# Kernel tuning notes

Measured on AMD Instinct MI355X. Metric: run time of the kernel, lower is better.

## Reference

```python
import jax, jax.numpy as jnp
import numpy as np

HIDDEN = 512
N_LAYERS = 2
SEQ = 512
BATCH = 64
H2 = HIDDEN * 2  # 1024
D_IN = H2 * (N_LAYERS + 1)  # 3072


def setup_inputs() -> dict:
    key = jax.random.key(0)
    ks = jax.random.split(key, 4)
    state = jax.random.normal(ks[0], (N_LAYERS, BATCH, H2), dtype=jnp.float32)
    encoder_output = jax.random.normal(ks[1], (SEQ, BATCH, H2), dtype=jnp.float32)
    # fc1: xavier_normal with tanh gain (5/3); fc2: kaiming_normal
    xavier_std = (5.0 / 3.0) * np.sqrt(2.0 / (D_IN + H2))
    W1 = jax.random.normal(ks[2], (H2, D_IN), dtype=jnp.float32) * xavier_std
    b1 = jnp.zeros((H2,), dtype=jnp.float32)
    W2 = jax.random.normal(ks[3], (1, H2), dtype=jnp.float32) * np.sqrt(2.0 / H2)
    b2 = jnp.zeros((1,), dtype=jnp.float32)
    return {"state": state, "encoder_output": encoder_output,
            "W1": W1, "b1": b1, "W2": W2, "b2": b2}


def reference(state, encoder_output, W1, b1, W2, b2):
    S, B, h2 = encoder_output.shape
    # (n_layers, B, H2) -> (B, n_layers*H2), broadcast over seq
    st = jnp.transpose(state, (1, 0, 2)).reshape(B, -1)
    st = jnp.broadcast_to(st[:, None, :], (B, S, st.shape[-1]))
    enc = jnp.transpose(encoder_output, (1, 0, 2))  # (B, S, H2)
    concat = jnp.concatenate([st, enc], axis=2)      # (B, S, 3*H2)
    energy = jnp.tanh(jnp.einsum('bsd,hd->bsh', concat, W1) + b1)
    energy = (jnp.einsum('bsh,oh->bso', energy, W2) + b2)  # (B, S, 1)
    energy = jnp.transpose(energy, (0, 2, 1))        # (B, 1, S)
    alpha = jax.nn.softmax(energy, axis=2)           # (B, 1, S)
    context = jnp.einsum('bqs,bsh->qbh', alpha, enc)  # (1, B, H2)
    return context, alpha
```

## Files before the change

kernel.cpp:

```cpp
#include <hip/hip_runtime.h>
#include <hip/hip_bf16.h>
#include <stdint.h>

#define H2      1024
#define SEQ     512
#define BATCH   64
#define M_TOTAL (SEQ * BATCH)

typedef __attribute__((ext_vector_type(8))) short short8;
typedef __attribute__((ext_vector_type(4))) float f32x4;

__device__ __forceinline__ unsigned pack2_bf16(float lo, float hi) {
    union { __hip_bfloat162 h; unsigned u; } v;
    v.h = __float22bfloat162_rn(make_float2(lo, hi));
    return v.u;
}

__device__ __forceinline__ float fast_tanh(float x) {
    float e = __expf(2.0f * x);
    return __fdividef(e - 1.0f, e + 1.0f);
}

__device__ __forceinline__ void gl_lds16(const unsigned short* g, unsigned short* l) {
    __builtin_amdgcn_global_load_lds(
        (const __attribute__((address_space(1))) unsigned int*)g,
        (__attribute__((address_space(3))) unsigned int*)l, 16, 0, 0);
}


__global__ __launch_bounds__(256) void k_setup(const float* __restrict__ W1,
                                               const float* __restrict__ b1,
                                               const float* __restrict__ state,
                                               const float* __restrict__ enc,
                                               unsigned short* __restrict__ W1e,
                                               unsigned short* __restrict__ encb,
                                               float* __restrict__ logits,
                                               float* __restrict__ sp) {
    __shared__ unsigned short T[16 * 512];
    int blk = blockIdx.x, tid = threadIdx.x;
    int lane = tid & 63;
    if (blk < 512) {
        int gr = blk * 4 + (tid >> 6);
        int h  = ((gr >> 5) << 4) + (lane & 15);
        int k  = ((gr & 31) << 5) + ((lane >> 4) << 3);
        const float* src = W1 + (size_t)h * 3072 + 2048 + k;
        float4 v0 = *(const float4*)(src);
        float4 v1 = *(const float4*)(src + 4);
        uint4 o;
        o.x = pack2_bf16(v0.x, v0.y); o.y = pack2_bf16(v0.z, v0.w);
        o.z = pack2_bf16(v1.x, v1.y); o.w = pack2_bf16(v1.z, v1.w);
        *(uint4*)(W1e + (size_t)gr * 512 + lane * 8) = o;
    } else if (blk < 640) {
        logits[(blk - 512) * 256 + tid] = 0.f;
    } else if (blk < 704) {
        int mT   = blk - 640;
        int wave = tid >> 6;
        int c    = lane & 15;
        int kq   = (lane >> 4) << 3;
        int h    = mT * 16 + c;
        int b    = wave * 16 + c;
        const float* ap = W1 + (size_t)h * 3072 + kq;
        f32x4 acc = {0.f, 0.f, 0.f, 0.f};
        #pragma unroll 4
        for (int k0 = 0; k0 < 2048; k0 += 32) {
            int k = k0 + kq;
            float4 a0 = *(const float4*)(ap + k0);
            float4 a1 = *(const float4*)(ap + k0 + 4);
            int l = k >> 10, j = k & 1023;
            const float* bp = state + (((size_t)l * 64 + b) << 10) + j;
            float4 b0 = *(const float4*)bp;
            float4 b1v = *(const float4*)(bp + 4);
            union { short8 s; uint4 u; } fa, fb;
            fa.u.x = pack2_bf16(a0.x, a0.y); fa.u.y = pack2_bf16(a0.z, a0.w);
            fa.u.z = pack2_bf16(a1.x, a1.y); fa.u.w = pack2_bf16(a1.z, a1.w);
            fb.u.x = pack2_bf16(b0.x, b0.y); fb.u.y = pack2_bf16(b0.z, b0.w);
            fb.u.z = pack2_bf16(b1v.x, b1v.y); fb.u.w = pack2_bf16(b1v.z, b1v.w);
            acc = __builtin_amdgcn_mfma_f32_16x16x32_bf16(fa.s, fb.s, acc, 0, 0, 0);
        }
        int quad = lane >> 4;
        int bcol = wave * 16 + c;
        #pragma unroll
        for (int i = 0; i < 4; ++i) {
            int hh = mT * 16 + quad * 4 + i;
            sp[((size_t)bcol << 10) + hh] = acc[i] + b1[hh];
        }
    } else {
        int RB = blk - 704;
        const float*    src = enc  + (size_t)RB * 16384;
        unsigned short* dst = encb + (size_t)RB * 16384;
        int rhalf = tid >> 7;
        int colq  = (tid & 127) << 2;
        #pragma unroll
        for (int h = 0; h < 2; ++h) {
            if (h) __syncthreads();
            #pragma unroll
            for (int rp = 0; rp < 8; ++rp) {
                int row = rp * 2 + rhalf;
                float4 v = *(const float4*)(src + (size_t)row * 1024 + h * 512 + colq);
                uint2 o;
                o.x = pack2_bf16(v.x, v.y);
                o.y = pack2_bf16(v.z, v.w);
                int byte = (row * 1024 + colq * 2) ^ ((row & 7) << 4);
                *(uint2*)((char*)T + byte) = o;
            }
            __syncthreads();
            #pragma unroll
            for (int q = 0; q < 4; ++q) {
                int c   = q * 256 + tid;
                int KCl = c >> 6;
                int L   = c & 63;
                int row = L & 15;
                int kb  = KCl * 64 + ((L >> 4) << 4);
                int byte = (row * 1024 + kb) ^ ((row & 7) << 4);
                uint4 d = *(const uint4*)((const char*)T + byte);
                *(uint4*)(dst + ((size_t)(h * 16 + KCl) * 512) + L * 8) = d;
            }
        }
    }
}

#define BM 128
#define BN 128
#define BK 64
#define KSTEPS (H2 / BK)

__global__ __launch_bounds__(256, 2) void k_energy(const unsigned short* __restrict__ encb,
                                                   const unsigned short* __restrict__ W1e,
                                                   const float* __restrict__ sp,
                                                   const float* __restrict__ W2,
                                                   float* __restrict__ logits) {
    __shared__ unsigned short As[BM * BK];
    __shared__ unsigned short Bs[BN * BK];
    int bid = blockIdx.x;
    int c8  = bid & 7;
    int jj  = bid >> 3;
    int mT  = c8 * 32 + (jj >> 3);
    int nT  = jj & 7;
    int n0  = nT * BN;
    int m0  = mT * BM;
    int tid  = threadIdx.x;
    int lane = tid & 63, wave = tid >> 6;
    int wm   = (wave >> 1) << 6;
    int wn   = (wave & 1) << 6;

    int rg0 = wave * 2, rg1 = wave * 2 + 1;
    const unsigned short* gA0 = encb + ((size_t)(mT * 8 + rg0) * 32) * 512 + lane * 8;
    const unsigned short* gA1 = encb + ((size_t)(mT * 8 + rg1) * 32) * 512 + lane * 8;
    const unsigned short* gB0 = W1e  + ((size_t)(nT * 8 + rg0) * 32) * 512 + lane * 8;
    const unsigned short* gB1 = W1e  + ((size_t)(nT * 8 + rg1) * 32) * 512 + lane * 8;
    unsigned short* lA00 = As + (rg0 * 2 + 0) * 512;
    unsigned short* lA01 = As + (rg0 * 2 + 1) * 512;
    unsigned short* lA10 = As + (rg1 * 2 + 0) * 512;
    unsigned short* lA11 = As + (rg1 * 2 + 1) * 512;
    unsigned short* lB00 = Bs + (rg0 * 2 + 0) * 512;
    unsigned short* lB01 = Bs + (rg0 * 2 + 1) * 512;
    unsigned short* lB10 = Bs + (rg1 * 2 + 0) * 512;
    unsigned short* lB11 = Bs + (rg1 * 2 + 1) * 512;

    f32x4 acc[4][4];
    #pragma unroll
    for (int mi = 0; mi < 4; ++mi)
        #pragma unroll
        for (int ni = 0; ni < 4; ++ni)
            acc[mi][ni] = (f32x4){0.f, 0.f, 0.f, 0.f};

    int ablk = wm >> 4;
    int bblk = wn >> 4;

    for (int t = 0; t < KSTEPS; ++t) {
        int go = t * 1024;
        __syncthreads();
        gl_lds16(gA0 + go,       lA00);
        gl_lds16(gA0 + go + 512, lA01);
        gl_lds16(gA1 + go,       lA10);
        gl_lds16(gA1 + go + 512, lA11);
        gl_lds16(gB0 + go,       lB00);
        gl_lds16(gB0 + go + 512, lB01);
        gl_lds16(gB1 + go,       lB10);
        gl_lds16(gB1 + go + 512, lB11);
        __syncthreads();
        short8 af[4][2], bf[4][2];
        #pragma unroll
        for (int i = 0; i < 4; ++i) {
            #pragma unroll
            for (int kh = 0; kh < 2; ++kh) {
                af[i][kh] = *(const short8*)(As + ((ablk + i) * 2 + kh) * 512 + lane * 8);
                bf[i][kh] = *(const short8*)(Bs + ((bblk + i) * 2 + kh) * 512 + lane * 8);
            }
        }
        #pragma unroll
        for (int mi = 0; mi < 4; ++mi)
            #pragma unroll
            for (int ni = 0; ni < 4; ++ni) {
                acc[mi][ni] = __builtin_amdgcn_mfma_f32_16x16x32_bf16(af[mi][0], bf[ni][0], acc[mi][ni], 0, 0, 0);
                acc[mi][ni] = __builtin_amdgcn_mfma_f32_16x16x32_bf16(af[mi][1], bf[ni][1], acc[mi][ni], 0, 0, 0);
            }
    }

    int c    = lane & 15;
    int quad = lane >> 4;
    float w2v[4];
    int   hcol[4];
    #pragma unroll
    for (int ni = 0; ni < 4; ++ni) {
        hcol[ni] = n0 + wn + ni * 16 + c;
        w2v[ni]  = W2[hcol[ni]];
    }
    #pragma unroll
    for (int mi = 0; mi < 4; ++mi) {
        #pragma unroll
        for (int i = 0; i < 4; ++i) {
            int m = m0 + wm + mi * 16 + quad * 4 + i;
            int b = m & 63;
            const float* sprow = sp + ((size_t)b << 10);
            float t = 0.f;
            #pragma unroll
            for (int ni = 0; ni < 4; ++ni) {
                float e = acc[mi][ni][i] + sprow[hcol[ni]];
                t = fmaf(fast_tanh(e), w2v[ni], t);
            }
            t += __shfl_xor(t, 1);
            t += __shfl_xor(t, 2);
            t += __shfl_xor(t, 4);
            t += __shfl_xor(t, 8);
            if (c == 0) atomicAdd(logits + (size_t)b * 512 + (m >> 6), t);
        }
    }
}

__global__ __launch_bounds__(256) void k_softmax(const float* __restrict__ logits,
                                                 float* __restrict__ alpha) {
    int b = blockIdx.x;
    int tid = threadIdx.x;
    int lane = tid & 63, wave = tid >> 6;
    float v0 = logits[(size_t)b * 512 + tid];
    float v1 = logits[(size_t)b * 512 + 256 + tid];
    float mx = fmaxf(v0, v1);
    #pragma unroll
    for (int o = 32; o; o >>= 1) mx = fmaxf(mx, __shfl_xor(mx, o));
    __shared__ float redm[4];
    if (lane == 0) redm[wave] = mx;
    __syncthreads();
    mx = fmaxf(fmaxf(redm[0], redm[1]), fmaxf(redm[2], redm[3]));
    float e0 = __expf(v0 - mx), e1 = __expf(v1 - mx);
    float s = e0 + e1;
    #pragma unroll
    for (int o = 32; o; o >>= 1) s += __shfl_xor(s, o);
    __shared__ float reds[4];
    if (lane == 0) reds[wave] = s;
    __syncthreads();
    s = reds[0] + reds[1] + reds[2] + reds[3];
    float inv = 1.0f / s;
    alpha[(size_t)b * 512 + tid]       = e0 * inv;
    alpha[(size_t)b * 512 + 256 + tid] = e1 * inv;
}

#define NSC 32
__global__ __launch_bounds__(256) void k_context(const float* __restrict__ enc,
                                                 const float* __restrict__ alpha,
                                                 float* __restrict__ part) {
    int b  = blockIdx.x & 63;
    int sc = blockIdx.x >> 6;
    int h  = threadIdx.x << 2;
    float4 acc = make_float4(0.f, 0.f, 0.f, 0.f);
    int sbase = sc * 16;
    #pragma unroll
    for (int si = 0; si < 16; ++si) {
        int s = sbase + si;
        float a = alpha[(size_t)b * 512 + s];
        float4 e = *(const float4*)(enc + (((size_t)s * 64 + b) << 10) + h);
        acc.x = fmaf(a, e.x, acc.x);
        acc.y = fmaf(a, e.y, acc.y);
        acc.z = fmaf(a, e.z, acc.z);
        acc.w = fmaf(a, e.w, acc.w);
    }
    *(float4*)(part + (((size_t)sc * 64 + b) << 10) + h) = acc;
}

__global__ __launch_bounds__(256) void k_reduce(const float* __restrict__ part,
                                                float* __restrict__ ctx) {
    int b = blockIdx.x;
    int h = threadIdx.x << 2;
    float4 acc = make_float4(0.f, 0.f, 0.f, 0.f);
    #pragma unroll
    for (int sc = 0; sc < NSC; ++sc) {
        float4 p = *(const float4*)(part + (((size_t)sc * 64 + b) << 10) + h);
        acc.x += p.x; acc.y += p.y; acc.z += p.z; acc.w += p.w;
    }
    *(float4*)(ctx + ((size_t)b << 10) + h) = acc;
}

extern "C" void kernel_launch(void* const* d_in, const int* in_sizes, int n_in,
                              void* d_out, int out_size, void* d_ws, size_t ws_size,
                              hipStream_t stream) {
    const float* state = (const float*)d_in[0];
    const float* enc   = (const float*)d_in[1];
    const float* W1    = (const float*)d_in[2];
    const float* b1    = (const float*)d_in[3];
    const float* W2    = (const float*)d_in[4];

    float* ctx   = (float*)d_out;
    float* alpha = (float*)d_out + 65536;

    char* ws = (char*)d_ws;
    unsigned short* W1e    = (unsigned short*)(ws);
    float*          sp     = (float*)(ws + 2097152);
    float*          logits = (float*)(ws + 2097152 + 262144);
    unsigned short* encb   = (unsigned short*)(ws + 2097152 + 262144 + 131072);
    float*          part   = (float*)encb;

    k_setup<<<704 + 2048, 256, 0, stream>>>(W1, b1, state, enc, W1e, encb,
                                            logits, sp);
    k_energy<<<M_TOTAL / BM * (H2 / BN), 256, 0, stream>>>(encb, W1e, sp, W2, logits);
    k_softmax<<<64, 256, 0, stream>>>(logits, alpha);
    k_context<<<NSC * 64, 256, 0, stream>>>(enc, alpha, part);
    k_reduce<<<64, 256, 0, stream>>>(part, ctx);
}
```

Before: 379.4 us.

## Fuse softmax, context and reduction into one kernel with atomic accumulation

Merges the softmax, context-partial and reduction kernels into a single kernel. Each block recomputes the per-batch max and sum from the logits and writes its slice of alpha. It then accumulates its context partial into ctx with float atomics; ctx is zeroed in the setup kernel. The encoder bf16 conversion is also restructured to load all 16 rows in one pass through a larger LDS tile instead of two halves. This drops two launches and the partial-buffer round trip, at the cost of redundant softmax reductions per block and many atomics.

```diff
diff --git a/kernel.cpp b/kernel.cpp
--- a/kernel.cpp
+++ b/kernel.cpp
@@ -35,8 +35,9 @@
                                                unsigned short* __restrict__ W1e,
                                                unsigned short* __restrict__ encb,
                                                float* __restrict__ logits,
-                                               float* __restrict__ sp) {
-    __shared__ unsigned short T[16 * 512];
+                                               float* __restrict__ sp,
+                                               float* __restrict__ ctx) {
+    __shared__ unsigned short T[16 * 1024];
     int blk = blockIdx.x, tid = threadIdx.x;
     int lane = tid & 63;
     if (blk < 512) {
@@ -52,6 +53,8 @@
         *(uint4*)(W1e + (size_t)gr * 512 + lane * 8) = o;
     } else if (blk < 640) {
         logits[(blk - 512) * 256 + tid] = 0.f;
+        int i = (blk - 512) * 512 + tid * 2;
+        *(float2*)(ctx + i) = make_float2(0.f, 0.f);
     } else if (blk < 704) {
         int mT   = blk - 640;
         int wave = tid >> 6;
@@ -88,33 +91,31 @@
         int RB = blk - 704;
         const float*    src = enc  + (size_t)RB * 16384;
         unsigned short* dst = encb + (size_t)RB * 16384;
-        int rhalf = tid >> 7;
-        int colq  = (tid & 127) << 2;
-        #pragma unroll
-        for (int h = 0; h < 2; ++h) {
-            if (h) __syncthreads();
-            #pragma unroll
-            for (int rp = 0; rp < 8; ++rp) {
-                int row = rp * 2 + rhalf;
-                float4 v = *(const float4*)(src + (size_t)row * 1024 + h * 512 + colq);
-                uint2 o;
-                o.x = pack2_bf16(v.x, v.y);
-                o.y = pack2_bf16(v.z, v.w);
-                int byte = (row * 1024 + colq * 2) ^ ((row & 7) << 4);
-                *(uint2*)((char*)T + byte) = o;
-            }
-            __syncthreads();
-            #pragma unroll
-            for (int q = 0; q < 4; ++q) {
-                int c   = q * 256 + tid;
-                int KCl = c >> 6;
-                int L   = c & 63;
-                int row = L & 15;
-                int kb  = KCl * 64 + ((L >> 4) << 4);
-                int byte = (row * 1024 + kb) ^ ((row & 7) << 4);
-                uint4 d = *(const uint4*)((const char*)T + byte);
-                *(uint4*)(dst + ((size_t)(h * 16 + KCl) * 512) + L * 8) = d;
-            }
+
+        float4 v[16];
+        #pragma unroll
+        for (int p = 0; p < 16; ++p)
+            v[p] = *(const float4*)(src + p * 1024 + (tid << 2));
+        #pragma unroll
+        for (int p = 0; p < 16; ++p) {
+            uint2 o;
+            o.x = pack2_bf16(v[p].x, v[p].y);
+            o.y = pack2_bf16(v[p].z, v[p].w);
+            int byte = (p * 2048 + (tid << 3)) ^ ((p & 7) << 4);
+            *(uint2*)((char*)T + byte) = o;
+        }
+        __syncthreads();
+
+        #pragma unroll
+        for (int q = 0; q < 8; ++q) {
+            int cchunk = q * 256 + tid;
+            int KC  = cchunk >> 6;
+            int L   = cchunk & 63;
+            int row = L & 15;
+            int kb  = KC * 64 + ((L >> 4) << 4);
+            int byte = (row * 2048 + kb) ^ ((row & 7) << 4);
+            uint4 d = *(const uint4*)((const char*)T + byte);
+            *(uint4*)(dst + (size_t)cchunk * 8) = d;
         }
     }
 }
@@ -228,66 +229,56 @@
     }
 }
 
-__global__ __launch_bounds__(256) void k_softmax(const float* __restrict__ logits,
-                                                 float* __restrict__ alpha) {
-    int b = blockIdx.x;
+__global__ __launch_bounds__(256) void k_ctx(const float* __restrict__ enc,
+                                             const float* __restrict__ logits,
+                                             float* __restrict__ alpha,
+                                             float* __restrict__ ctx) {
+    __shared__ float lg[512];
+    __shared__ float redm[4], reds[4];
+    int b   = blockIdx.x & 63;
+    int sc  = blockIdx.x >> 6;
     int tid = threadIdx.x;
     int lane = tid & 63, wave = tid >> 6;
+
     float v0 = logits[(size_t)b * 512 + tid];
     float v1 = logits[(size_t)b * 512 + 256 + tid];
+    lg[tid]       = v0;
+    lg[tid + 256] = v1;
     float mx = fmaxf(v0, v1);
     #pragma unroll
     for (int o = 32; o; o >>= 1) mx = fmaxf(mx, __shfl_xor(mx, o));
-    __shared__ float redm[4];
     if (lane == 0) redm[wave] = mx;
     __syncthreads();
     mx = fmaxf(fmaxf(redm[0], redm[1]), fmaxf(redm[2], redm[3]));
-    float e0 = __expf(v0 - mx), e1 = __expf(v1 - mx);
-    float s = e0 + e1;
+    float s = __expf(v0 - mx) + __expf(v1 - mx);
     #pragma unroll
     for (int o = 32; o; o >>= 1) s += __shfl_xor(s, o);
-    __shared__ float reds[4];
     if (lane == 0) reds[wave] = s;
     __syncthreads();
     s = reds[0] + reds[1] + reds[2] + reds[3];
     float inv = 1.0f / s;
-    alpha[(size_t)b * 512 + tid]       = e0 * inv;
-    alpha[(size_t)b * 512 + 256 + tid] = e1 * inv;
-}
-
-#define NSC 32
-__global__ __launch_bounds__(256) void k_context(const float* __restrict__ enc,
-                                                 const float* __restrict__ alpha,
-                                                 float* __restrict__ part) {
-    int b  = blockIdx.x & 63;
-    int sc = blockIdx.x >> 6;
-    int h  = threadIdx.x << 2;
+
+    int sbase = sc * 16;
+    if (tid < 16)
+        alpha[(size_t)b * 512 + sbase + tid] = __expf(lg[sbase + tid] - mx) * inv;
+
+    int h = tid << 2;
     float4 acc = make_float4(0.f, 0.f, 0.f, 0.f);
-    int sbase = sc * 16;
     #pragma unroll
     for (int si = 0; si < 16; ++si) {
-        int s = sbase + si;
-        float a = alpha[(size_t)b * 512 + s];
-        float4 e = *(const float4*)(enc + (((size_t)s * 64 + b) << 10) + h);
+        int sidx = sbase + si;
+        float a = __expf(lg[sidx] - mx) * inv;
+        float4 e = *(const float4*)(enc + (((size_t)sidx * 64 + b) << 10) + h);
         acc.x = fmaf(a, e.x, acc.x);
         acc.y = fmaf(a, e.y, acc.y);
         acc.z = fmaf(a, e.z, acc.z);
         acc.w = fmaf(a, e.w, acc.w);
     }
-    *(float4*)(part + (((size_t)sc * 64 + b) << 10) + h) = acc;
-}
-
-__global__ __launch_bounds__(256) void k_reduce(const float* __restrict__ part,
-                                                float* __restrict__ ctx) {
-    int b = blockIdx.x;
-    int h = threadIdx.x << 2;
-    float4 acc = make_float4(0.f, 0.f, 0.f, 0.f);
-    #pragma unroll
-    for (int sc = 0; sc < NSC; ++sc) {
-        float4 p = *(const float4*)(part + (((size_t)sc * 64 + b) << 10) + h);
-        acc.x += p.x; acc.y += p.y; acc.z += p.z; acc.w += p.w;
-    }
-    *(float4*)(ctx + ((size_t)b << 10) + h) = acc;
+    float* dst = ctx + ((size_t)b << 10) + h;
+    atomicAdd(dst + 0, acc.x);
+    atomicAdd(dst + 1, acc.y);
+    atomicAdd(dst + 2, acc.z);
+    atomicAdd(dst + 3, acc.w);
 }
 
 extern "C" void kernel_launch(void* const* d_in, const int* in_sizes, int n_in,
@@ -307,12 +298,9 @@
     float*          sp     = (float*)(ws + 2097152);
     float*          logits = (float*)(ws + 2097152 + 262144);
     unsigned short* encb   = (unsigned short*)(ws + 2097152 + 262144 + 131072);
-    float*          part   = (float*)encb;
 
     k_setup<<<704 + 2048, 256, 0, stream>>>(W1, b1, state, enc, W1e, encb,
-                                            logits, sp);
+                                            logits, sp, ctx);
     k_energy<<<M_TOTAL / BM * (H2 / BN), 256, 0, stream>>>(encb, W1e, sp, W2, logits);
-    k_softmax<<<64, 256, 0, stream>>>(logits, alpha);
-    k_context<<<NSC * 64, 256, 0, stream>>>(enc, alpha, part);
-    k_reduce<<<64, 256, 0, stream>>>(part, ctx);
-}
+    k_ctx<<<32 * 64, 256, 0, stream>>>(enc, logits, alpha, ctx);
+}
```

Result: faster. 354.2 us (-6.6%).

## Fuse encoder bf16 conversion into energy GEMM loading fp32 tiles directly

Applied to the files above, without the earlier changes.

Removes the setup pass that converted the encoder output to a bf16 tiled copy. The energy GEMM now streams fp32 encoder rows into LDS through a swizzled layout with direct global-to-LDS loads, then converts to bf16 while building MFMA fragments. This saves one full read and write of the 128MB encoder tensor. In exchange each GEMM block reads twice the A bytes from global memory, across all 8 N tiles, and does extra conversion work in the inner loop.

```diff
diff --git a/kernel.cpp b/kernel.cpp
--- a/kernel.cpp
+++ b/kernel.cpp
@@ -26,17 +26,19 @@
         (const __attribute__((address_space(1))) unsigned int*)g,
         (__attribute__((address_space(3))) unsigned int*)l, 16, 0, 0);
 }
+__device__ __forceinline__ void gl_lds16f(const float* g, float* l) {
+    __builtin_amdgcn_global_load_lds(
+        (const __attribute__((address_space(1))) unsigned int*)g,
+        (__attribute__((address_space(3))) unsigned int*)l, 16, 0, 0);
+}
 
 
 __global__ __launch_bounds__(256) void k_setup(const float* __restrict__ W1,
                                                const float* __restrict__ b1,
                                                const float* __restrict__ state,
-                                               const float* __restrict__ enc,
                                                unsigned short* __restrict__ W1e,
-                                               unsigned short* __restrict__ encb,
                                                float* __restrict__ logits,
                                                float* __restrict__ sp) {
-    __shared__ unsigned short T[16 * 512];
     int blk = blockIdx.x, tid = threadIdx.x;
     int lane = tid & 63;
     if (blk < 512) {
@@ -52,7 +54,7 @@
         *(uint4*)(W1e + (size_t)gr * 512 + lane * 8) = o;
     } else if (blk < 640) {
         logits[(blk - 512) * 256 + tid] = 0.f;
-    } else if (blk < 704) {
+    } else {
         int mT   = blk - 640;
         int wave = tid >> 6;
         int c    = lane & 15;
@@ -84,38 +86,6 @@
             int hh = mT * 16 + quad * 4 + i;
             sp[((size_t)bcol << 10) + hh] = acc[i] + b1[hh];
         }
-    } else {
-        int RB = blk - 704;
-        const float*    src = enc  + (size_t)RB * 16384;
-        unsigned short* dst = encb + (size_t)RB * 16384;
-        int rhalf = tid >> 7;
-        int colq  = (tid & 127) << 2;
-        #pragma unroll
-        for (int h = 0; h < 2; ++h) {
-            if (h) __syncthreads();
-            #pragma unroll
-            for (int rp = 0; rp < 8; ++rp) {
-                int row = rp * 2 + rhalf;
-                float4 v = *(const float4*)(src + (size_t)row * 1024 + h * 512 + colq);
-                uint2 o;
-                o.x = pack2_bf16(v.x, v.y);
-                o.y = pack2_bf16(v.z, v.w);
-                int byte = (row * 1024 + colq * 2) ^ ((row & 7) << 4);
-                *(uint2*)((char*)T + byte) = o;
-            }
-            __syncthreads();
-            #pragma unroll
-            for (int q = 0; q < 4; ++q) {
-                int c   = q * 256 + tid;
-                int KCl = c >> 6;
-                int L   = c & 63;
-                int row = L & 15;
-                int kb  = KCl * 64 + ((L >> 4) << 4);
-                int byte = (row * 1024 + kb) ^ ((row & 7) << 4);
-                uint4 d = *(const uint4*)((const char*)T + byte);
-                *(uint4*)(dst + ((size_t)(h * 16 + KCl) * 512) + L * 8) = d;
-            }
-        }
     }
 }
 
@@ -124,12 +94,12 @@
 #define BK 64
 #define KSTEPS (H2 / BK)
 
-__global__ __launch_bounds__(256, 2) void k_energy(const unsigned short* __restrict__ encb,
+__global__ __launch_bounds__(256, 2) void k_energy(const float* __restrict__ enc,
                                                    const unsigned short* __restrict__ W1e,
                                                    const float* __restrict__ sp,
                                                    const float* __restrict__ W2,
                                                    float* __restrict__ logits) {
-    __shared__ unsigned short As[BM * BK];
+    __shared__ float          Af[8 * 1024];
     __shared__ unsigned short Bs[BN * BK];
     int bid = blockIdx.x;
     int c8  = bid & 7;
@@ -142,16 +112,22 @@
     int lane = tid & 63, wave = tid >> 6;
     int wm   = (wave >> 1) << 6;
     int wn   = (wave & 1) << 6;
+    int q    = lane >> 4;
 
     int rg0 = wave * 2, rg1 = wave * 2 + 1;
-    const unsigned short* gA0 = encb + ((size_t)(mT * 8 + rg0) * 32) * 512 + lane * 8;
-    const unsigned short* gA1 = encb + ((size_t)(mT * 8 + rg1) * 32) * 512 + lane * 8;
-    const unsigned short* gB0 = W1e  + ((size_t)(nT * 8 + rg0) * 32) * 512 + lane * 8;
-    const unsigned short* gB1 = W1e  + ((size_t)(nT * 8 + rg1) * 32) * 512 + lane * 8;
-    unsigned short* lA00 = As + (rg0 * 2 + 0) * 512;
-    unsigned short* lA01 = As + (rg0 * 2 + 1) * 512;
-    unsigned short* lA10 = As + (rg1 * 2 + 0) * 512;
-    unsigned short* lA11 = As + (rg1 * 2 + 1) * 512;
+    const float* gA[2][4];
+    #pragma unroll
+    for (int rr = 0; rr < 2; ++rr) {
+        int rg = wave * 2 + rr;
+        #pragma unroll
+        for (int j = 0; j < 4; ++j) {
+            int r  = 4 * j + q;
+            int kp = (lane & 15) ^ (r & 7);
+            gA[rr][j] = enc + (size_t)(m0 + rg * 16 + r) * 1024 + kp * 4;
+        }
+    }
+    const unsigned short* gB0 = W1e + ((size_t)(nT * 8 + rg0) * 32) * 512 + lane * 8;
+    const unsigned short* gB1 = W1e + ((size_t)(nT * 8 + rg1) * 32) * 512 + lane * 8;
     unsigned short* lB00 = Bs + (rg0 * 2 + 0) * 512;
     unsigned short* lB01 = Bs + (rg0 * 2 + 1) * 512;
     unsigned short* lB10 = Bs + (rg1 * 2 + 0) * 512;
@@ -166,14 +142,18 @@
 
     int ablk = wm >> 4;
     int bblk = wn >> 4;
+    int row  = lane & 15;
+    int r7   = row & 7;
 
     for (int t = 0; t < KSTEPS; ++t) {
         int go = t * 1024;
+        int ao = t * BK;
         __syncthreads();
-        gl_lds16(gA0 + go,       lA00);
-        gl_lds16(gA0 + go + 512, lA01);
-        gl_lds16(gA1 + go,       lA10);
-        gl_lds16(gA1 + go + 512, lA11);
+        #pragma unroll
+        for (int rr = 0; rr < 2; ++rr)
+            #pragma unroll
+            for (int j = 0; j < 4; ++j)
+                gl_lds16f(gA[rr][j] + ao, Af + (wave * 2 + rr) * 1024 + j * 256);
         gl_lds16(gB0 + go,       lB00);
         gl_lds16(gB0 + go + 512, lB01);
         gl_lds16(gB1 + go,       lB10);
@@ -182,9 +162,16 @@
         short8 af[4][2], bf[4][2];
         #pragma unroll
         for (int i = 0; i < 4; ++i) {
+            const float* areg = Af + (ablk + i) * 1024 + row * 64;
             #pragma unroll
             for (int kh = 0; kh < 2; ++kh) {
-                af[i][kh] = *(const short8*)(As + ((ablk + i) * 2 + kh) * 512 + lane * 8);
+                int kp0 = kh * 8 + 2 * q;
+                float4 f0 = *(const float4*)(areg + ((kp0 ^ r7) << 2));
+                float4 f1 = *(const float4*)(areg + (((kp0 + 1) ^ r7) << 2));
+                union { short8 s; uint4 u; } fa;
+                fa.u.x = pack2_bf16(f0.x, f0.y); fa.u.y = pack2_bf16(f0.z, f0.w);
+                fa.u.z = pack2_bf16(f1.x, f1.y); fa.u.w = pack2_bf16(f1.z, f1.w);
+                af[i][kh] = fa.s;
                 bf[i][kh] = *(const short8*)(Bs + ((bblk + i) * 2 + kh) * 512 + lane * 8);
             }
         }
@@ -306,12 +293,10 @@
     unsigned short* W1e    = (unsigned short*)(ws);
     float*          sp     = (float*)(ws + 2097152);
     float*          logits = (float*)(ws + 2097152 + 262144);
-    unsigned short* encb   = (unsigned short*)(ws + 2097152 + 262144 + 131072);
-    float*          part   = (float*)encb;
-
-    k_setup<<<704 + 2048, 256, 0, stream>>>(W1, b1, state, enc, W1e, encb,
-                                            logits, sp);
-    k_energy<<<M_TOTAL / BM * (H2 / BN), 256, 0, stream>>>(encb, W1e, sp, W2, logits);
+    float*          part   = (float*)(ws + 2097152 + 262144 + 131072);
+
+    k_setup<<<704, 256, 0, stream>>>(W1, b1, state, W1e, logits, sp);
+    k_energy<<<M_TOTAL / BM * (H2 / BN), 256, 0, stream>>>(enc, W1e, sp, W2, logits);
     k_softmax<<<64, 256, 0, stream>>>(logits, alpha);
     k_context<<<NSC * 64, 256, 0, stream>>>(enc, alpha, part);
     k_reduce<<<64, 256, 0, stream>>>(part, ctx);
```

Result: slower. 402.4 us (+6.1%).
